# Performance work log

Hardware: AMD Instinct MI355X
Metric: run time of the kernel (lower is better)

The kernel has to match this reference:

```python
import jax, jax.numpy as jnp
import numpy as np
from jax import lax

W_BCE, W_DICE, W_FT, W_HD = 1.0, 1.0, 1.0, 0.1
TV_ALPHA, TV_BETA, TV_GAMMA = 0.7, 0.3, 0.75
HD_MAX_DIST, HD_BK = 10, 3
SMOOTH, EPS, HD_EPS = 1e-6, 1e-7, 1e-8


def _max_pool(x, k):
    # torch F.max_pool2d pads with -inf implicitly
    pad = k // 2
    return lax.reduce_window(x, -jnp.inf, lax.max, (1, 1, k, k), (1, 1, 1, 1),
                             [(0, 0), (0, 0), (pad, pad), (pad, pad)])


def _min_pool(x, k):
    pad = k // 2
    return lax.reduce_window(x, jnp.inf, lax.min, (1, 1, k, k), (1, 1, 1, 1),
                             [(0, 0), (0, 0), (pad, pad), (pad, pad)])


def _soft_boundary(mask, k):
    dil = _max_pool(mask, k)
    ero = _min_pool(mask, k)  # == -max_pool(-mask)
    return jnp.maximum(dil - ero, 0.0)


def _bce_with_logits(logits, target):
    # numerically stable: max(x,0) - x*t + log1p(exp(-|x|))
    return jnp.mean(jnp.maximum(logits, 0.0) - logits * target +
                    jnp.log1p(jnp.exp(-jnp.abs(logits))))


def _dice_loss(probs, target):
    p = probs.reshape(probs.shape[0], -1)
    t = target.reshape(target.shape[0], -1)
    inter = jnp.sum(p * t, axis=1)
    denom = jnp.sum(p, axis=1) + jnp.sum(t, axis=1)
    dice = (2.0 * inter + SMOOTH) / (denom + SMOOTH + EPS)
    return jnp.mean(1.0 - dice)


def _focal_tversky(probs, target):
    p = probs.reshape(probs.shape[0], -1)
    t = target.reshape(target.shape[0], -1)
    TP = jnp.sum(p * t, axis=1)
    FP = jnp.sum(p * (1.0 - t), axis=1)
    FN = jnp.sum((1.0 - p) * t, axis=1)
    tv = (TP + SMOOTH) / (TP + TV_ALPHA * FP + TV_BETA * FN + SMOOTH + EPS)
    return jnp.mean(jnp.power(1.0 - tv, TV_GAMMA))


def _hausdorff_surrogate(probs, target):
    pred_b = _soft_boundary(probs, HD_BK)
    gt_b = _soft_boundary(target, HD_BK)
    total = jnp.zeros((), probs.dtype)
    weight_sum = 0.0
    for d in range(1, HD_MAX_DIST + 1):
        pred_d = _max_pool(pred_b, 2 * d + 1)
        gt_d = _max_pool(gt_b, 2 * d + 1)
        w = float(d) / float(HD_MAX_DIST)
        total = total + w * (jnp.mean(jnp.abs(pred_d - gt_b)) +
                             jnp.mean(jnp.abs(gt_d - pred_b)))
        weight_sum += w
    return total / (weight_sum + HD_EPS)


def setup_inputs() -> dict:
    key = jax.random.key(0)
    k1, k2 = jax.random.split(key)
    B, C, H, W = 16, 1, 512, 512
    logits = jax.random.normal(k1, (B, C, H, W), dtype=jnp.float32)
    target = jax.random.randint(k2, (B, C, H, W), 0, 2, dtype=jnp.int32)
    return {"logits": logits, "target": target}


def reference(logits, target):
    t = target.astype(jnp.float32)
    bce = _bce_with_logits(logits, t)
    probs = jax.nn.sigmoid(logits)
    d = _dice_loss(probs, t)
    ft = _focal_tversky(probs, t)
    hd = _hausdorff_surrogate(probs, t)
    return W_BCE * bce + W_DICE * d + W_FT * ft + W_HD * hd
```

## Files before the change

### kernel.cpp

```cpp
#include <hip/hip_runtime.h>
#include <math.h>

namespace {

constexpr int B = 16, H = 512, W = 512;
constexpr int HWc = H * W;
constexpr size_t Nc = (size_t)B * HWc;

constexpr int NSTRIP = 13;
constexpr int CENT = 42;
constexpr int NBAND = 16;
constexpr int NWORK = NSTRIP * NBAND * B * 2;
constexpr int NSB = NWORK / 4;
constexpr int NBCE = B * 64;


template <int CTRL>
__device__ __forceinline__ float dpp_shift1(float v) {
  int i = __float_as_int(v);
  int r = __builtin_amdgcn_update_dpp(i, i, CTRL, 0xF, 0xF, false);
  return __int_as_float(r);
}
template <int CTRL>
__device__ __forceinline__ unsigned dpp_shift1u(unsigned v) {
  return (unsigned)__builtin_amdgcn_update_dpp((int)v, (int)v, CTRL, 0xF, 0xF,
                                               false);
}

__device__ __forceinline__ float hmax3(float v) {
  return fmaxf(fmaxf(dpp_shift1<0x138>(v), v), dpp_shift1<0x130>(v));
}
__device__ __forceinline__ void hminmax3(float v, float& mx, float& mn) {
  float s1 = dpp_shift1<0x138>(v);
  float s2 = dpp_shift1<0x130>(v);
  mx = fmaxf(fmaxf(s1, v), s2);
  mn = fminf(fminf(s1, v), s2);
}

__device__ __forceinline__ unsigned long long or3_lanes(unsigned long long v) {
  unsigned lo = (unsigned)v, hi = (unsigned)(v >> 32);
  unsigned rlo = dpp_shift1u<0x138>(lo) | lo | dpp_shift1u<0x130>(lo);
  unsigned rhi = dpp_shift1u<0x138>(hi) | hi | dpp_shift1u<0x130>(hi);
  return ((unsigned long long)rhi << 32) | rlo;
}
__device__ __forceinline__ unsigned long long and3_lanes(unsigned long long v) {
  unsigned lo = (unsigned)v, hi = (unsigned)(v >> 32);
  unsigned rlo = dpp_shift1u<0x138>(lo) & lo & dpp_shift1u<0x130>(lo);
  unsigned rhi = dpp_shift1u<0x138>(hi) & hi & dpp_shift1u<0x130>(hi);
  return ((unsigned long long)rhi << 32) | rlo;
}

__device__ __forceinline__ float wave_sum(float v) {
#pragma unroll
  for (int off = 32; off > 0; off >>= 1) v += __shfl_down(v, off);
  return v;
}

__device__ __forceinline__ float block_reduce_256(float v, float* sm, int tid) {
#pragma unroll
  for (int off = 32; off > 0; off >>= 1) v += __shfl_down(v, off);
  int lane = tid & 63, wid = tid >> 6;
  if (lane == 0) sm[wid] = v;
  __syncthreads();
  float r = 0.f;
  if (tid == 0) r = sm[0] + sm[1] + sm[2] + sm[3];
  __syncthreads();
  return r;
}

template <int CH>
__device__ __forceinline__ float load_src(const float* __restrict__ Lg,
                                          const int* __restrict__ Tg, int gy,
                                          int colc) {
  gy = min(max(gy, 0), H - 1);
  if constexpr (CH == 0) {
    float x = Lg[gy * W + colc];
    float e = __expf(-x);
    return __builtin_amdgcn_rcpf(1.f + e);
  } else {
    return (float)Tg[gy * W + colc];
  }
}

template <int D>
__device__ __forceinline__ void dilate_steps(float (&a)[52],
                                             const float (&o)[32],
                                             float (&accv)[4]) {
  if constexpr (D <= 10) {
    float hp = hmax3(a[D - 1]);
    float hc = hmax3(a[D]);
#pragma unroll
    for (int r = D; r <= 51 - D; ++r) {
      float hn = hmax3(a[r + 1]);
      float nv = fmaxf(fmaxf(hp, hc), hn);
      hp = hc;
      hc = hn;
      a[r] = nv;
    }
    constexpr float wd = 0.1f * (float)D;
#pragma unroll
    for (int k = 0; k < 32; ++k) accv[k & 3] += wd * fabsf(a[10 + k] - o[k]);
    dilate_steps<D + 1>(a, o, accv);
  }
}

__device__ __forceinline__ void fused_body0(const float* __restrict__ Lg,
                                            const int* __restrict__ Tg,
                                            int lane, int strip, int band,
                                            int bz,
                                            float* __restrict__ chain_p) {
  int col = strip * CENT - 11 + lane;
  int colc = min(max(col, 0), W - 1);
  int y0 = band * 32;

  float o[32];
  {
    float v0 = load_src<1>(Lg, Tg, y0 - 1, colc);
    float v1 = load_src<1>(Lg, Tg, y0, colc);
    float hx0, hn0, hx1, hn1;
    hminmax3(v0, hx0, hn0);
    hminmax3(v1, hx1, hn1);
#pragma unroll
    for (int k = 0; k < 32; ++k) {
      float v2 = load_src<1>(Lg, Tg, y0 + 1 + k, colc);
      float hx2, hn2;
      hminmax3(v2, hx2, hn2);
      o[k] = fmaxf(fmaxf(hx0, hx1), hx2) - fminf(fminf(hn0, hn1), hn2);
      hx0 = hx1;
      hx1 = hx2;
      hn0 = hn1;
      hn1 = hn2;
    }
  }

  float a[52];
  {
    float v0 = load_src<0>(Lg, Tg, y0 - 11, colc);
    float v1 = load_src<0>(Lg, Tg, y0 - 10, colc);
    float hx0, hn0, hx1, hn1;
    hminmax3(v0, hx0, hn0);
    hminmax3(v1, hx1, hn1);
#pragma unroll
    for (int r = 0; r < 52; ++r) {
      float v2 = load_src<0>(Lg, Tg, y0 - 9 + r, colc);
      float hx2, hn2;
      hminmax3(v2, hx2, hn2);
      a[r] = fmaxf(fmaxf(hx0, hx1), hx2) - fminf(fminf(hn0, hn1), hn2);
      hx0 = hx1;
      hx1 = hx2;
      hn0 = hn1;
      hn1 = hn2;
    }
  }

  float accv[4] = {0.f, 0.f, 0.f, 0.f};
  dilate_steps<1>(a, o, accv);
  float acc = (accv[0] + accv[1]) + (accv[2] + accv[3]);

  bool valid = (lane >= 11 && lane <= 52 && col < W);
  acc = valid ? acc : 0.f;
  acc = wave_sum(acc);
  if (lane == 0) chain_p[(bz * NBAND + band) * NSTRIP + strip] = acc;
}

__device__ __forceinline__ void fused_body1(const float* __restrict__ Lg,
                                            const int* __restrict__ Tg,
                                            int lane, int strip, int band,
                                            int bz,
                                            float* __restrict__ chain_p) {
  int col = strip * CENT - 11 + lane;
  int colc = min(max(col, 0), W - 1);
  int y0 = band * 32;

  float o[32];
  {
    float v0 = load_src<0>(Lg, Tg, y0 - 1, colc);
    float v1 = load_src<0>(Lg, Tg, y0, colc);
    float hx0, hn0, hx1, hn1;
    hminmax3(v0, hx0, hn0);
    hminmax3(v1, hx1, hn1);
#pragma unroll
    for (int k = 0; k < 32; ++k) {
      float v2 = load_src<0>(Lg, Tg, y0 + 1 + k, colc);
      float hx2, hn2;
      hminmax3(v2, hx2, hn2);
      o[k] = fmaxf(fmaxf(hx0, hx1), hx2) - fminf(fminf(hn0, hn1), hn2);
      hx0 = hx1;
      hx1 = hx2;
      hn0 = hn1;
      hn1 = hn2;
    }
  }

  unsigned long long tb = 0ull;
#pragma unroll
  for (int j = 0; j < 54; ++j) {
    int gy = min(max(y0 - 11 + j, 0), H - 1);
    tb |= (unsigned long long)(unsigned)Tg[gy * W + colc] << j;
  }

  unsigned long long vd = tb | (tb << 1) | (tb >> 1);
  unsigned long long ve = tb & (tb << 1) & (tb >> 1);
  unsigned long long ab = (or3_lanes(vd) & ~and3_lanes(ve)) >> 1;

  unsigned long long p0 = 0ull, p1 = 0ull, p2 = 0ull, p3 = 0ull;
#pragma unroll
  for (int d = 1; d <= 10; ++d) {
    unsigned long long s = ab | (ab << 1) | (ab >> 1);
    ab = or3_lanes(s);
    unsigned long long carry = ab, t;
    t = p0 & carry;
    p0 ^= carry;
    carry = t;
    t = p1 & carry;
    p1 ^= carry;
    carry = t;
    t = p2 & carry;
    p2 ^= carry;
    carry = t;
    p3 ^= carry;
  }

  float accv[4] = {0.f, 0.f, 0.f, 0.f};
  {
    unsigned l0 = (unsigned)p0, h0 = (unsigned)(p0 >> 32);
    unsigned l1 = (unsigned)p1, h1 = (unsigned)(p1 >> 32);
    unsigned l2 = (unsigned)p2, h2 = (unsigned)(p2 >> 32);
    unsigned l3 = (unsigned)p3, h3 = (unsigned)(p3 >> 32);
#pragma unroll
    for (int k = 0; k < 32; ++k) {
      unsigned c;
      if (k < 22) {
        const int i = 10 + k;
        c = ((l0 >> i) & 1u) | (((l1 >> i) & 1u) << 1) |
            (((l2 >> i) & 1u) << 2) | (((l3 >> i) & 1u) << 3);
      } else {
        const int i = k - 22;
        c = ((h0 >> i) & 1u) | (((h1 >> i) & 1u) << 1) |
            (((h2 >> i) & 1u) << 2) | (((h3 >> i) & 1u) << 3);
      }
      float cf = (float)c;
      float S = 0.05f * cf * (21.f - cf);
      accv[k & 3] += S + o[k] * (5.5f - 2.f * S);
    }
  }
  float acc = (accv[0] + accv[1]) + (accv[2] + accv[3]);

  bool valid = (lane >= 11 && lane <= 52 && col < W);
  acc = valid ? acc : 0.f;
  acc = wave_sum(acc);
  if (lane == 0) chain_p[(bz * NBAND + band) * NSTRIP + strip] = acc;
}

__device__ __forceinline__ void bce_body(const float* __restrict__ logits,
                                         const int* __restrict__ target,
                                         int blk, float* __restrict__ bceA,
                                         float* __restrict__ spA,
                                         float* __restrict__ stA,
                                         float* __restrict__ sptA, float* sm) {
  int img = blk >> 6, seg = blk & 63;
  const float4* L4 =
      (const float4*)(logits + (size_t)img * HWc + (size_t)seg * 4096);
  const int4* T4 =
      (const int4*)(target + (size_t)img * HWc + (size_t)seg * 4096);
  int tid = threadIdx.x;
  float s_bce = 0.f, s_p = 0.f, s_t = 0.f, s_pt = 0.f;
#pragma unroll
  for (int it = 0; it < 4; ++it) {
    float4 x4 = L4[it * 256 + tid];
    int4 t4 = T4[it * 256 + tid];
    float xs[4] = {x4.x, x4.y, x4.z, x4.w};
    int ts[4] = {t4.x, t4.y, t4.z, t4.w};
#pragma unroll
    for (int j = 0; j < 4; ++j) {
      float x = xs[j];
      float tf = (float)ts[j];
      float e = __expf(-x);
      float p = __builtin_amdgcn_rcpf(1.f + e);
      s_p += p;
      s_t += tf;
      s_pt += p * tf;
      s_bce += x * (1.f - tf) + __logf(1.f + e);
    }
  }
  float r;
  r = block_reduce_256(s_bce, sm, tid);
  if (tid == 0) bceA[blk] = r;
  r = block_reduce_256(s_p, sm, tid);
  if (tid == 0) spA[blk] = r;
  r = block_reduce_256(s_t, sm, tid);
  if (tid == 0) stA[blk] = r;
  r = block_reduce_256(s_pt, sm, tid);
  if (tid == 0) sptA[blk] = r;
}

__global__ void __launch_bounds__(256, 4) fused_kernel(
    const float* __restrict__ logits, const int* __restrict__ target,
    float* __restrict__ bceA, float* __restrict__ spA,
    float* __restrict__ stA, float* __restrict__ sptA,
    float* __restrict__ chain_p) {
  __shared__ float smr[4];
  int tid = threadIdx.x;
  if (blockIdx.x < NBCE) {
    bce_body(logits, target, blockIdx.x, bceA, spA, stA, sptA, smr);
    return;
  }
  int lane = tid & 63;
  int wv = __builtin_amdgcn_readfirstlane(tid >> 6);
  int widx = (blockIdx.x - NBCE) * 4 + wv;
  int strip = widx % NSTRIP;
  int rest = widx / NSTRIP;
  int band = rest & 15;
  int bz = rest >> 4;
  int img = bz & 15, chain = bz >> 4;
  const float* Lg = logits + (size_t)img * HWc;
  const int* Tg = target + (size_t)img * HWc;
  if (chain == 0)
    fused_body0(Lg, Tg, lane, strip, band, bz, chain_p);
  else
    fused_body1(Lg, Tg, lane, strip, band, bz, chain_p);
}

__global__ void finalize_kernel(const float* __restrict__ bceA,
                                const float* __restrict__ spA,
                                const float* __restrict__ stA,
                                const float* __restrict__ sptA,
                                const float* __restrict__ chain_p,
                                float* __restrict__ out) {
  __shared__ float smr[4];
  __shared__ float smImg[16][3];
  __shared__ double smd[16][2];
  int tid = threadIdx.x;

  float s = 0.f;
  {
    const float4* b4 = (const float4*)bceA;
    for (int i = tid; i < NBCE / 4; i += 256) {
      float4 v = b4[i];
      s += (v.x + v.y) + (v.z + v.w);
    }
  }
  float bce_sum = block_reduce_256(s, smr, tid);

  s = 0.f;
  {
    const float4* c4 = (const float4*)chain_p;
    for (int i = tid; i < NWORK / 4; i += 256) {
      float4 v = c4[i];
      s += (v.x + v.y) + (v.z + v.w);
    }
  }
  float hd_sum = block_reduce_256(s, smr, tid);

  {
    int img = tid >> 4, part = tid & 15;
    float sp = 0.f, st = 0.f, spt = 0.f;
    for (int j = part; j < 64; j += 16) {
      int idx = img * 64 + j;
      sp += spA[idx];
      st += stA[idx];
      spt += sptA[idx];
    }
#pragma unroll
    for (int off = 8; off > 0; off >>= 1) {
      sp += __shfl_down(sp, off, 16);
      st += __shfl_down(st, off, 16);
      spt += __shfl_down(spt, off, 16);
    }
    if (part == 0) {
      smImg[img][0] = sp;
      smImg[img][1] = st;
      smImg[img][2] = spt;
    }
  }
  __syncthreads();
  if (tid < 16) {
    double sp = smImg[tid][0], st = smImg[tid][1], spt = smImg[tid][2];
    double dice = (2.0 * spt + 1e-6) / (sp + st + 1e-6 + 1e-7);
    double tv = (spt + 1e-6) /
                (spt + 0.7 * (sp - spt) + 0.3 * (st - spt) + 1e-6 + 1e-7);
    smd[tid][0] = 1.0 - dice;
    smd[tid][1] = pow(1.0 - tv, 0.75);
  }
  __syncthreads();
  if (tid == 0) {
    double dice_l = 0.0, ft_l = 0.0;
    for (int i = 0; i < 16; ++i) {
      dice_l += smd[i][0];
      ft_l += smd[i][1];
    }
    dice_l /= 16.0;
    ft_l /= 16.0;
    const double Nd = (double)Nc;
    double bce = (double)bce_sum / Nd;
    double hd = ((double)hd_sum / Nd) / (5.5 + 1e-8);
    out[0] = (float)(bce + dice_l + ft_l + 0.1 * hd);
  }
}

}

extern "C" void kernel_launch(void* const* d_in, const int* in_sizes, int n_in,
                              void* d_out, int out_size, void* d_ws,
                              size_t ws_size, hipStream_t stream) {
  const float* logits = (const float*)d_in[0];
  const int* target = (const int*)d_in[1];
  float* out = (float*)d_out;

  float* part = (float*)d_ws;
  float* bceA = part;
  float* spA = part + NBCE;
  float* stA = part + 2 * NBCE;
  float* sptA = part + 3 * NBCE;
  float* chain_p = part + 4 * NBCE;

  fused_kernel<<<dim3(NBCE + NSB), dim3(256), 0, stream>>>(
      logits, target, bceA, spA, stA, sptA, chain_p);
  finalize_kernel<<<1, 256, 0, stream>>>(bceA, spA, stA, sptA, chain_p, out);
}
```

Baseline: 114.3 us.

## Use binary gt-boundary sign trick and co-schedule both chains per block

```diff
diff --git a/kernel.cpp b/kernel.cpp
--- a/kernel.cpp
+++ b/kernel.cpp
@@ -10,7 +10,8 @@
 constexpr int NSTRIP = 13;
 constexpr int CENT = 42;
 constexpr int NBAND = 16;
-constexpr int NWORK = NSTRIP * NBAND * B * 2;
+constexpr int NCELL = NSTRIP * NBAND * B;
+constexpr int NWORK = NCELL * 2;
 constexpr int NSB = NWORK / 4;
 constexpr int NBCE = B * 64;
 
@@ -68,23 +69,17 @@
   return r;
 }
 
-template <int CH>
-__device__ __forceinline__ float load_src(const float* __restrict__ Lg,
-                                          const int* __restrict__ Tg, int gy,
-                                          int colc) {
+__device__ __forceinline__ float sigmoid_at(const float* __restrict__ Lg,
+                                            int gy, int colc) {
   gy = min(max(gy, 0), H - 1);
-  if constexpr (CH == 0) {
-    float x = Lg[gy * W + colc];
-    float e = __expf(-x);
-    return __builtin_amdgcn_rcpf(1.f + e);
-  } else {
-    return (float)Tg[gy * W + colc];
-  }
+  float x = Lg[gy * W + colc];
+  float e = __expf(-x);
+  return __builtin_amdgcn_rcpf(1.f + e);
 }
 
 template <int D>
 __device__ __forceinline__ void dilate_steps(float (&a)[52],
-                                             const float (&o)[32],
+                                             const float (&sa)[32],
                                              float (&accv)[4]) {
   if constexpr (D <= 10) {
     float hp = hmax3(a[D - 1]);
@@ -99,8 +94,8 @@
     }
     constexpr float wd = 0.1f * (float)D;
 #pragma unroll
-    for (int k = 0; k < 32; ++k) accv[k & 3] += wd * fabsf(a[10 + k] - o[k]);
-    dilate_steps<D + 1>(a, o, accv);
+    for (int k = 0; k < 32; ++k) accv[k & 3] += wd * (sa[k] * a[10 + k]);
+    dilate_steps<D + 1>(a, sa, accv);
   }
 }
 
@@ -113,36 +108,33 @@
   int colc = min(max(col, 0), W - 1);
   int y0 = band * 32;
 
-  float o[32];
-  {
-    float v0 = load_src<1>(Lg, Tg, y0 - 1, colc);
-    float v1 = load_src<1>(Lg, Tg, y0, colc);
+  unsigned gtmask;
+  {
+    unsigned long long tb = 0ull;
+#pragma unroll
+    for (int j = 0; j < 34; ++j) {
+      int gy = min(max(y0 - 1 + j, 0), H - 1);
+      tb |= (unsigned long long)(unsigned)Tg[gy * W + colc] << j;
+    }
+    unsigned long long vd = tb | (tb << 1) | (tb >> 1);
+    unsigned long long ve = tb & (tb << 1) & (tb >> 1);
+    gtmask = (unsigned)(((or3_lanes(vd) & ~and3_lanes(ve)) >> 1) &
+                        0xFFFFFFFFull);
+  }
+  float sa[32];
+#pragma unroll
+  for (int k = 0; k < 32; ++k) sa[k] = ((gtmask >> k) & 1u) ? -1.f : 1.f;
+
+  float a[52];
+  {
+    float v0 = sigmoid_at(Lg, y0 - 11, colc);
+    float v1 = sigmoid_at(Lg, y0 - 10, colc);
     float hx0, hn0, hx1, hn1;
     hminmax3(v0, hx0, hn0);
     hminmax3(v1, hx1, hn1);
 #pragma unroll
-    for (int k = 0; k < 32; ++k) {
-      float v2 = load_src<1>(Lg, Tg, y0 + 1 + k, colc);
-      float hx2, hn2;
-      hminmax3(v2, hx2, hn2);
-      o[k] = fmaxf(fmaxf(hx0, hx1), hx2) - fminf(fminf(hn0, hn1), hn2);
-      hx0 = hx1;
-      hx1 = hx2;
-      hn0 = hn1;
-      hn1 = hn2;
-    }
-  }
-
-  float a[52];
-  {
-    float v0 = load_src<0>(Lg, Tg, y0 - 11, colc);
-    float v1 = load_src<0>(Lg, Tg, y0 - 10, colc);
-    float hx0, hn0, hx1, hn1;
-    hminmax3(v0, hx0, hn0);
-    hminmax3(v1, hx1, hn1);
-#pragma unroll
     for (int r = 0; r < 52; ++r) {
-      float v2 = load_src<0>(Lg, Tg, y0 - 9 + r, colc);
+      float v2 = sigmoid_at(Lg, y0 - 9 + r, colc);
       float hx2, hn2;
       hminmax3(v2, hx2, hn2);
       a[r] = fmaxf(fmaxf(hx0, hx1), hx2) - fminf(fminf(hn0, hn1), hn2);
@@ -154,8 +146,9 @@
   }
 
   float accv[4] = {0.f, 0.f, 0.f, 0.f};
-  dilate_steps<1>(a, o, accv);
+  dilate_steps<1>(a, sa, accv);
   float acc = (accv[0] + accv[1]) + (accv[2] + accv[3]);
+  acc += 5.5f * (float)__popc(gtmask);
 
   bool valid = (lane >= 11 && lane <= 52 && col < W);
   acc = valid ? acc : 0.f;
@@ -174,14 +167,14 @@
 
   float o[32];
   {
-    float v0 = load_src<0>(Lg, Tg, y0 - 1, colc);
-    float v1 = load_src<0>(Lg, Tg, y0, colc);
+    float v0 = sigmoid_at(Lg, y0 - 1, colc);
+    float v1 = sigmoid_at(Lg, y0, colc);
     float hx0, hn0, hx1, hn1;
     hminmax3(v0, hx0, hn0);
     hminmax3(v1, hx1, hn1);
 #pragma unroll
     for (int k = 0; k < 32; ++k) {
-      float v2 = load_src<0>(Lg, Tg, y0 + 1 + k, colc);
+      float v2 = sigmoid_at(Lg, y0 + 1 + k, colc);
       float hx2, hn2;
       hminmax3(v2, hx2, hn2);
       o[k] = fmaxf(fmaxf(hx0, hx1), hx2) - fminf(fminf(hn0, hn1), hn2);
@@ -307,18 +300,19 @@
   }
   int lane = tid & 63;
   int wv = __builtin_amdgcn_readfirstlane(tid >> 6);
-  int widx = (blockIdx.x - NBCE) * 4 + wv;
-  int strip = widx % NSTRIP;
-  int rest = widx / NSTRIP;
+  int sb = blockIdx.x - NBCE;
+  int cell = sb * 2 + (wv & 1);
+  int chain = wv >> 1;
+  int strip = cell % NSTRIP;
+  int rest = cell / NSTRIP;
   int band = rest & 15;
-  int bz = rest >> 4;
-  int img = bz & 15, chain = bz >> 4;
+  int img = rest >> 4;
   const float* Lg = logits + (size_t)img * HWc;
   const int* Tg = target + (size_t)img * HWc;
   if (chain == 0)
-    fused_body0(Lg, Tg, lane, strip, band, bz, chain_p);
+    fused_body0(Lg, Tg, lane, strip, band, img, chain_p);
   else
-    fused_body1(Lg, Tg, lane, strip, band, bz, chain_p);
+    fused_body1(Lg, Tg, lane, strip, band, 16 + img, chain_p);
 }
 
 __global__ void finalize_kernel(const float* __restrict__ bceA,
```

Measured after the change: 146.2 us. 1.28x slower.
